# Performance work log

Hardware: AMD Instinct MI355X
Metric: run time of the kernel (lower is better)

Reference implementation:

```python
import jax, jax.numpy as jnp
import numpy as np

# Module hyperparams (from init_kwargs)
B, C, F, K, H, W = 8, 32, 32, 3, 32, 32
Q = K * K          # kernel positions
PAD = K // 2       # 'same' padding (output spatial == input spatial)
# groups = in_channels (num_groups=None default) -> step = 1, weight axis = F*Q*C


def setup_inputs() -> dict:
    key = jax.random.key(0)
    k1, k2, k3 = jax.random.split(key, 3)
    x = jax.random.normal(k1, (B, C, H, W), dtype=jnp.float32)
    # learned per-weight rational coefficients: one rational per (f, kernel_pos, channel)
    nums = jax.random.normal(k2, (F * Q * C, 6), dtype=jnp.float32) * 0.1
    denoms = jax.random.normal(k3, (F * Q * C, 4), dtype=jnp.float32) * 0.1
    return {"x": x, "nums": nums, "denoms": denoms}


def reference(x, nums, denoms):
    # per-weight Pade rational activation over conv windows, scatter-accumulated
    # into output channels:
    #   out[b,f,y,x] = sum_{q in KxK, c} P_{f,q,c}(w) / (1 + |D_{f,q,c}(w)|),
    #   w = zero-padded input at window position q, channel c.
    a = nums.reshape(F, Q, C, 6)    # numerator coeffs, powers 0..5
    b = denoms.reshape(F, Q, C, 4)  # denominator coeffs, powers 1..4

    xp = jnp.pad(x, ((0, 0), (0, 0), (PAD, PAD), (PAD, PAD)))
    # gather K*K shifted views: [B, C, Q, H, W]
    win = jnp.stack([xp[:, :, i:i + H, j:j + W]
                     for i in range(K) for j in range(K)], axis=2)

    # powers w^0..w^5: [B, C, Q, 6, H, W]
    w1 = win
    w2 = w1 * w1
    w3 = w2 * w1
    w4 = w2 * w2
    w5 = w4 * w1
    pows = jnp.stack([jnp.ones_like(w1), w1, w2, w3, w4, w5], axis=3)

    # numerator P and denominator D, per (f, q, c): [B, F, Q, C, H, W]
    num = jnp.einsum('bcqphw,fqcp->bfqchw', pows, a)
    den = 1.0 + jnp.abs(jnp.einsum('bcqphw,fqcp->bfqchw', pows[:, :, :, 1:5], b))

    # accumulate over kernel positions and channels -> [B, F, H, W]
    return jnp.sum(num / den, axis=(2, 3))
```

## Files before the change

### kernel.cpp

```cpp
#include <hip/hip_runtime.h>
#include <math.h>

#define NB 8
#define NC 32
#define NF 32
#define NH 32
#define NW 32
#define NQ 9
#define FSPLIT 8
#define FPB 4

__global__ __launch_bounds__(256, 8) void ka_conv_rational_kernel(
    const float* __restrict__ x,
    const float* __restrict__ nums,
    const float* __restrict__ dens,
    float* __restrict__ out)
{
    __shared__ float xt[NC][3][NW + 2];

    const int t   = threadIdx.x;
    const int bid = blockIdx.x;
    const int fq  = bid & (FSPLIT - 1);
    const int y   = (bid >> 3) & (NH - 1);
    const int b   = bid >> 8;

#pragma unroll
    for (int i = 0; i < 12; ++i) {
        int e   = t + i * 256;
        int c   = e >> 5;
        int ri  = c - (c / 3) * 3;
        (void)ri;
        int cc  = e / 96;
        int rem = e - cc * 96;
        int rr  = rem >> 5;
        int col = rem & 31;
        int gy  = y - 1 + rr;
        float v = (gy >= 0 && gy < NH)
                      ? x[(((size_t)b * NC + cc) * NH + gy) * NW + col]
                      : 0.f;
        xt[cc][rr][col + 1] = v;
    }
    if (t < 96) {
        int cc = t / 3, rr = t - (t / 3) * 3;
        xt[cc][rr][0] = 0.f;
    } else if (t >= 128 && t < 224) {
        int u = t - 128;
        int cc = u / 3, rr = u - (u / 3) * 3;
        xt[cc][rr][33] = 0.f;
    }
    __syncthreads();

    const int lane = t & 63;
    const int c    = lane & 31;
    const int sl   = lane >> 5;
    const int wv   = t >> 6;
    const int f    = fq * FPB + wv;

    const float* __restrict__ nbase = nums + ((size_t)f * NQ * NC + c) * 6;
    const float* __restrict__ dbase = dens + ((size_t)f * NQ * NC + c) * 4;

    float acc[16];
#pragma unroll
    for (int i = 0; i < 16; ++i) acc[i] = 0.f;

    float A0 = nbase[0], A1 = nbase[1], A2 = nbase[2],
          A3 = nbase[3], A4 = nbase[4], A5 = nbase[5];
    float D0 = dbase[0], D1 = dbase[1], D2 = dbase[2], D3 = dbase[3];

#pragma unroll 1
    for (int q = 0; q < NQ; ++q) {
        const float a0 = A0, a1 = A1, a2 = A2, a3 = A3, a4 = A4, a5 = A5;
        const float d0 = D0, d1 = D1, d2 = D2, d3 = D3;
        if (q + 1 < NQ) {
            const float* nn = nbase + (size_t)(q + 1) * NC * 6;
            const float* dn = dbase + (size_t)(q + 1) * NC * 4;
            A0 = nn[0]; A1 = nn[1]; A2 = nn[2];
            A3 = nn[3]; A4 = nn[4]; A5 = nn[5];
            D0 = dn[0]; D1 = dn[1]; D2 = dn[2]; D3 = dn[3];
        }
        const int qi = q / 3, qj = q - qi * 3;
        const float* wrow = &xt[c][qi][qj + sl];

#pragma unroll
        for (int it = 0; it < 16; ++it) {
            float w  = wrow[it * 2];
            float nu = fmaf(a5, w, a4);
            nu = fmaf(nu, w, a3);
            nu = fmaf(nu, w, a2);
            nu = fmaf(nu, w, a1);
            nu = fmaf(nu, w, a0);
            float dd = fmaf(d3, w, d2);
            dd = fmaf(dd, w, d1);
            dd = fmaf(dd, w, d0);
            dd *= w;
            float de = 1.0f + fabsf(dd);
            acc[it] = fmaf(nu, __builtin_amdgcn_rcpf(de), acc[it]);
        }
    }

#pragma unroll
    for (int it = 0; it < 16; ++it) {
        float v = acc[it];
        v += __shfl_xor(v, 1, 64);
        v += __shfl_xor(v, 2, 64);
        v += __shfl_xor(v, 4, 64);
        v += __shfl_xor(v, 8, 64);
        v += __shfl_xor(v, 16, 64);
        acc[it] = v;
    }

    float* op = out + (((size_t)b * NF + f) * NH + y) * NW;
#pragma unroll
    for (int it = 0; it < 16; ++it)
        if (c == it)
            op[it * 2 + sl] = acc[it];
}

extern "C" void kernel_launch(void* const* d_in, const int* in_sizes, int n_in,
                              void* d_out, int out_size, void* d_ws, size_t ws_size,
                              hipStream_t stream) {
    const float* x    = (const float*)d_in[0];
    const float* nums = (const float*)d_in[1];
    const float* dens = (const float*)d_in[2];
    float* out = (float*)d_out;

    dim3 grid(NB * NH * FSPLIT);
    dim3 block(256);
    ka_conv_rational_kernel<<<grid, block, 0, stream>>>(x, nums, dens, out);
}
```

Measured before the change: 85.66 us.

## Give each half-wave a contiguous column block and reuse row windows across kernel columns

Each half-wave now owns a contiguous 16-column half of the output row instead of interleaved columns. Each thread processes it in two groups of 8 columns, loading a 10-element window per kernel row with vectorized LDS loads (float4, float4, float2) and reusing it for all three horizontal kernel offsets. Coefficient loads become float2 vector loads issued per kernel position, replacing the software-prefetched scalar loads. The change is meant to cut LDS load instructions and halve the accumulator registers. In exchange it loses the coefficient prefetch, so global or cache latency may now be exposed, and the shuffle reductions stay at 16 per thread.

Result: slower. 100.0 us (+16.8%).

```diff
diff --git a/kernel.cpp b/kernel.cpp
--- a/kernel.cpp
+++ b/kernel.cpp
@@ -9,6 +9,9 @@
 #define NQ 9
 #define FSPLIT 8
 #define FPB 4
+#define TSX 36
+
+typedef float f2 __attribute__((ext_vector_type(2)));
 
 __global__ __launch_bounds__(256, 8) void ka_conv_rational_kernel(
     const float* __restrict__ x,
@@ -16,7 +19,7 @@
     const float* __restrict__ dens,
     float* __restrict__ out)
 {
-    __shared__ float xt[NC][3][NW + 2];
+    __shared__ float xt[NC][3][TSX];
 
     const int t   = threadIdx.x;
     const int bid = blockIdx.x;
@@ -27,9 +30,6 @@
 #pragma unroll
     for (int i = 0; i < 12; ++i) {
         int e   = t + i * 256;
-        int c   = e >> 5;
-        int ri  = c - (c / 3) * 3;
-        (void)ri;
         int cc  = e / 96;
         int rem = e - cc * 96;
         int rr  = rem >> 5;
@@ -56,64 +56,66 @@
     const int wv   = t >> 6;
     const int f    = fq * FPB + wv;
 
-    const float* __restrict__ nbase = nums + ((size_t)f * NQ * NC + c) * 6;
-    const float* __restrict__ dbase = dens + ((size_t)f * NQ * NC + c) * 4;
-
-    float acc[16];
-#pragma unroll
-    for (int i = 0; i < 16; ++i) acc[i] = 0.f;
-
-    float A0 = nbase[0], A1 = nbase[1], A2 = nbase[2],
-          A3 = nbase[3], A4 = nbase[4], A5 = nbase[5];
-    float D0 = dbase[0], D1 = dbase[1], D2 = dbase[2], D3 = dbase[3];
+    const float* __restrict__ nb = nums + ((size_t)f * NQ * NC + c) * 6;
+    const float* __restrict__ db = dens + ((size_t)f * NQ * NC + c) * 4;
+    float* __restrict__ op = out + (((size_t)b * NF + f) * NH + y) * NW;
 
 #pragma unroll 1
-    for (int q = 0; q < NQ; ++q) {
-        const float a0 = A0, a1 = A1, a2 = A2, a3 = A3, a4 = A4, a5 = A5;
-        const float d0 = D0, d1 = D1, d2 = D2, d3 = D3;
-        if (q + 1 < NQ) {
-            const float* nn = nbase + (size_t)(q + 1) * NC * 6;
-            const float* dn = dbase + (size_t)(q + 1) * NC * 4;
-            A0 = nn[0]; A1 = nn[1]; A2 = nn[2];
-            A3 = nn[3]; A4 = nn[4]; A5 = nn[5];
-            D0 = dn[0]; D1 = dn[1]; D2 = dn[2]; D3 = dn[3];
-        }
-        const int qi = q / 3, qj = q - qi * 3;
-        const float* wrow = &xt[c][qi][qj + sl];
+    for (int g = 0; g < 2; ++g) {
+        float acc[8];
+#pragma unroll
+        for (int j = 0; j < 8; ++j) acc[j] = 0.f;
+
+#pragma unroll 1
+        for (int qi = 0; qi < 3; ++qi) {
+            const float* wp = &xt[c][qi][(sl << 4) + (g << 3)];
+            float4 wA = *(const float4*)wp;
+            float4 wB = *(const float4*)(wp + 4);
+            f2     wC = *(const f2*)(wp + 8);
+            const float w[10] = {wA.x, wA.y, wA.z, wA.w,
+                                 wB.x, wB.y, wB.z, wB.w,
+                                 wC.x, wC.y};
 
 #pragma unroll
-        for (int it = 0; it < 16; ++it) {
-            float w  = wrow[it * 2];
-            float nu = fmaf(a5, w, a4);
-            nu = fmaf(nu, w, a3);
-            nu = fmaf(nu, w, a2);
-            nu = fmaf(nu, w, a1);
-            nu = fmaf(nu, w, a0);
-            float dd = fmaf(d3, w, d2);
-            dd = fmaf(dd, w, d1);
-            dd = fmaf(dd, w, d0);
-            dd *= w;
-            float de = 1.0f + fabsf(dd);
-            acc[it] = fmaf(nu, __builtin_amdgcn_rcpf(de), acc[it]);
+            for (int qj = 0; qj < 3; ++qj) {
+                const float* ap = nb + (size_t)(qi * 3 + qj) * NC * 6;
+                const float* bp = db + (size_t)(qi * 3 + qj) * NC * 4;
+                f2 A01 = *(const f2*)ap;
+                f2 A23 = *(const f2*)(ap + 2);
+                f2 A45 = *(const f2*)(ap + 4);
+                f2 D01 = *(const f2*)bp;
+                f2 D23 = *(const f2*)(bp + 2);
+
+#pragma unroll
+                for (int j = 0; j < 8; ++j) {
+                    float ww = w[j + qj];
+                    float nu = fmaf(A45.y, ww, A45.x);
+                    nu = fmaf(nu, ww, A23.y);
+                    nu = fmaf(nu, ww, A23.x);
+                    nu = fmaf(nu, ww, A01.y);
+                    nu = fmaf(nu, ww, A01.x);
+                    float dd = fmaf(D23.y, ww, D23.x);
+                    dd = fmaf(dd, ww, D01.y);
+                    dd = fmaf(dd, ww, D01.x);
+                    dd *= ww;
+                    float de = 1.0f + fabsf(dd);
+                    acc[j] = fmaf(nu, __builtin_amdgcn_rcpf(de), acc[j]);
+                }
+            }
+        }
+
+#pragma unroll
+        for (int j = 0; j < 8; ++j) {
+            float v = acc[j];
+            v += __shfl_xor(v, 1);
+            v += __shfl_xor(v, 2);
+            v += __shfl_xor(v, 4);
+            v += __shfl_xor(v, 8);
+            v += __shfl_xor(v, 16);
+            if (c == (g << 3) + j)
+                op[(sl << 4) + (g << 3) + j] = v;
         }
     }
-
-#pragma unroll
-    for (int it = 0; it < 16; ++it) {
-        float v = acc[it];
-        v += __shfl_xor(v, 1, 64);
-        v += __shfl_xor(v, 2, 64);
-        v += __shfl_xor(v, 4, 64);
-        v += __shfl_xor(v, 8, 64);
-        v += __shfl_xor(v, 16, 64);
-        acc[it] = v;
-    }
-
-    float* op = out + (((size_t)b * NF + f) * NH + y) * NW;
-#pragma unroll
-    for (int it = 0; it < 16; ++it)
-        if (c == it)
-            op[it * 2 + sl] = acc[it];
 }
 
 extern "C" void kernel_launch(void* const* d_in, const int* in_sizes, int n_in,
```
